# Optimization experiments

Measured on AMD Instinct MI355X. Metric: run time of the kernel, lower is better.

## Reference

```python
import jax, jax.numpy as jnp
import numpy as np

D_G, D_2D, D_3D = 512, 768, 1024
D_F, RANK, ATTN_H = 256, 16, 512
B = 8192


def _xavier(key, shape):
    fan_out, fan_in = shape
    lim = float(np.sqrt(6.0 / (fan_in + fan_out)))
    return jax.random.uniform(key, shape, jnp.float32, -lim, lim)


def setup_inputs() -> dict:
    key = jax.random.key(0)
    ks = jax.random.split(key, 12)
    inp = {
        "h_g": jax.random.normal(ks[0], (B, D_G), jnp.float32),
        "h_2d": jax.random.normal(ks[1], (B, D_2D), jnp.float32),
        "h_3d": jax.random.normal(ks[2], (B, D_3D), jnp.float32),
        # modality projections (torch Linear: y = x @ W.T + b)
        "Wg": _xavier(ks[3], (D_F, D_G)),   "bg": jnp.zeros((D_F,), jnp.float32),
        "W2": _xavier(ks[4], (D_F, D_2D)),  "b2": jnp.zeros((D_F,), jnp.float32),
        "W3": _xavier(ks[5], (D_F, D_3D)),  "b3": jnp.zeros((D_F,), jnp.float32),
        # LayerNorm affine params
        "ln_g_w": jnp.ones((D_F,), jnp.float32),  "ln_g_b": jnp.zeros((D_F,), jnp.float32),
        "ln_2_w": jnp.ones((D_F,), jnp.float32),  "ln_2_b": jnp.zeros((D_F,), jnp.float32),
        "ln_3_w": jnp.ones((D_F,), jnp.float32),  "ln_3_b": jnp.zeros((D_F,), jnp.float32),
        # rank expansions (no bias)
        "U": _xavier(ks[6], (RANK * D_F, D_F)),
        "V": _xavier(ks[7], (RANK * D_F, D_F)),
        "S": _xavier(ks[8], (RANK * D_F, D_F)),
        # attention MLP
        "Wa1": _xavier(ks[9], (ATTN_H, D_G + D_2D + D_3D)), "ba1": jnp.zeros((ATTN_H,), jnp.float32),
        "Wa2": _xavier(ks[10], (RANK, ATTN_H)),             "ba2": jnp.zeros((RANK,), jnp.float32),
    }
    return inp


def _layernorm(x, w, b, eps=1e-5):
    mu = jnp.mean(x, axis=-1, keepdims=True)
    var = jnp.var(x, axis=-1, keepdims=True)
    return (x - mu) * jax.lax.rsqrt(var + eps) * w + b


def reference(h_g, h_2d, h_3d, Wg, bg, W2, b2, W3, b3,
              ln_g_w, ln_g_b, ln_2_w, ln_2_b, ln_3_w, ln_3_b,
              U, V, S, Wa1, ba1, Wa2, ba2):
    # proj + LN + ReLU (dropout=0 / eval mode)
    g = jax.nn.relu(_layernorm(h_g @ Wg.T + bg, ln_g_w, ln_g_b))
    d2 = jax.nn.relu(_layernorm(h_2d @ W2.T + b2, ln_2_w, ln_2_b))
    d3 = jax.nn.relu(_layernorm(h_3d @ W3.T + b3, ln_3_w, ln_3_b))
    b = g.shape[0]
    # rank expansion: (B, R, d_f)
    g_r = (g @ U.T).reshape(b, RANK, D_F)
    d2_r = (d2 @ V.T).reshape(b, RANK, D_F)
    d3_r = (d3 @ S.T).reshape(b, RANK, D_F)
    z_r = g_r * d2_r * d3_r  # elementwise tri-linear product
    # rank attention from raw modality concat
    h_cat = jnp.concatenate([h_g, h_2d, h_3d], axis=-1)
    beta = jax.nn.softmax(jax.nn.relu(h_cat @ Wa1.T + ba1) @ Wa2.T + ba2, axis=-1)  # (B, R)
    z = jnp.einsum('brd,br->bd', z_r, beta)  # (B, d_f)
    return z
```

## Files before the change

kernel.cpp:

```cpp
#include <hip/hip_runtime.h>
#include <stdint.h>

#define B_ROWS 8192
#define DG 512
#define D2 768
#define D3 1024
#define DCAT 2304
#define DF 256
#define RANK 16
#define AH 512

#define OFF_WG 0
#define OFF_W2 131072
#define OFF_W3 327680
#define OFF_U  589824
#define OFF_V  1638400
#define OFF_S  2686976
#define OFF_WA1 3735552

#define WS_WBUF  0u
#define WS_HCAT  9830400u
#define WS_GBUF  9830400u
#define WS_PROJ  47579136u
#define WS_A1ACC 72744960u
#define WS_BETA  89522176u
#define WS_ZPART 47579136u
#define WS_REQUIRED 94240768u

typedef __attribute__((ext_vector_type(8))) short short8;
typedef __attribute__((ext_vector_type(4))) float f32x4;

__device__ inline unsigned short f2bf(float f) {
  union { float f; unsigned int u; } v; v.f = f;
  unsigned int u = v.u + 0x7fffu + ((v.u >> 16) & 1u);
  return (unsigned short)(u >> 16);
}
__device__ inline float bf2f(unsigned short h) {
  union { float f; unsigned int u; } v; v.u = ((unsigned int)h) << 16;
  return v.f;
}

typedef const unsigned int __attribute__((address_space(1)))* as1_u32p;
typedef unsigned int __attribute__((address_space(3)))* as3_u32p;

__device__ inline void g2l16(const unsigned short* g, unsigned short* l) {
  __builtin_amdgcn_global_load_lds((as1_u32p)g, (as3_u32p)l, 16, 0, 0);
}


__global__ __launch_bounds__(256) void cvt_hcat_k(const float* __restrict__ hg,
                                                  const float* __restrict__ h2,
                                                  const float* __restrict__ h3,
                                                  unsigned short* __restrict__ hcat) {
  const int idx = blockIdx.x * 256 + threadIdx.x;
  const int e = idx * 4;
  const int row = e / DCAT;
  const int col = e - row * DCAT;
  const float* src;
  if (col < DG) src = hg + (size_t)row * DG + col;
  else if (col < DG + D2) src = h2 + (size_t)row * D2 + (col - DG);
  else src = h3 + (size_t)row * D3 + (col - DG - D2);
  float4 v = *(const float4*)src;
  ushort4 o;
  o.x = f2bf(v.x); o.y = f2bf(v.y); o.z = f2bf(v.z); o.w = f2bf(v.w);
  *(ushort4*)(hcat + e) = o;
}

__global__ __launch_bounds__(256) void cvt_weights_k(const float* __restrict__ Wg,
                                                     const float* __restrict__ W2,
                                                     const float* __restrict__ W3,
                                                     const float* __restrict__ U,
                                                     const float* __restrict__ V,
                                                     const float* __restrict__ S,
                                                     const float* __restrict__ Wa1,
                                                     unsigned short* __restrict__ wbuf) {
  const int idx = blockIdx.x * 256 + threadIdx.x;
  const int e = idx * 4;
  const float* src;
  if (e < OFF_W2)       src = Wg  + e;
  else if (e < OFF_W3)  src = W2  + (e - OFF_W2);
  else if (e < OFF_U)   src = W3  + (e - OFF_W3);
  else if (e < OFF_V)   src = U   + (e - OFF_U);
  else if (e < OFF_S)   src = V   + (e - OFF_V);
  else if (e < OFF_WA1) src = S   + (e - OFF_S);
  else                  src = Wa1 + (e - OFF_WA1);
  float4 v = *(const float4*)src;
  ushort4 o;
  o.x = f2bf(v.x); o.y = f2bf(v.y); o.z = f2bf(v.z); o.w = f2bf(v.w);
  *(ushort4*)(wbuf + e) = o;
}


__device__ __forceinline__ void gemm_mainloop(const unsigned short* Ag, int lda,
                                              const unsigned short* Bg, int ldb,
                                              int K,
                                              unsigned short* lA, unsigned short* lB,
                                              f32x4 acc[4][4]) {
  const int tid = threadIdx.x;
  const int lane = tid & 63;
  const int wr = tid >> 7;
  const int wc = (tid >> 6) & 1;
#pragma unroll
  for (int i = 0; i < 4; ++i)
#pragma unroll
    for (int j = 0; j < 4; ++j)
      acc[i][j] = (f32x4){0.f, 0.f, 0.f, 0.f};

  const int row_s = tid >> 3;
  const int kc_s = (((tid & 7) ^ ((tid >> 3) & 7)) << 3);
  const int mbase = wr * 64 + (lane & 15);
  const int nbase = wc * 64 + (lane & 15);
  const int kq = lane >> 4;
  const int h = lane & 7;

  const int nsteps = K >> 6;
  for (int ks = 0; ks < nsteps; ++ks) {
    const int k0 = ks << 6;
    __syncthreads();
#pragma unroll
    for (int p = 0; p < 4; ++p) {
      const int row = p * 32 + row_s;
      const int lofs = (p * 256 + tid) * 8;
      g2l16(Ag + (size_t)row * lda + k0 + kc_s, lA + lofs);
      g2l16(Bg + (size_t)row * ldb + k0 + kc_s, lB + lofs);
    }
    __syncthreads();
#pragma unroll
    for (int kk = 0; kk < 2; ++kk) {
      const int kch = (kk << 2) + kq;
      const int ko = ((kch ^ h) << 3);
      short8 af[4], bfr[4];
#pragma unroll
      for (int t = 0; t < 4; ++t) {
        af[t]  = *(const short8*)(lA + (mbase + t * 16) * 64 + ko);
        bfr[t] = *(const short8*)(lB + (nbase + t * 16) * 64 + ko);
      }
#pragma unroll
      for (int ti = 0; ti < 4; ++ti)
#pragma unroll
        for (int tj = 0; tj < 4; ++tj)
          acc[ti][tj] = __builtin_amdgcn_mfma_f32_16x16x32_bf16(af[ti], bfr[tj], acc[ti][tj], 0, 0, 0);
    }
  }
}


__global__ __launch_bounds__(256) void fatgemm_k(const unsigned short* __restrict__ hcat,
                                                 const unsigned short* __restrict__ wbuf,
                                                 float* __restrict__ proj,
                                                 float* __restrict__ a1acc) {
  __shared__ __align__(16) unsigned short lA[128 * 64];
  __shared__ __align__(16) unsigned short lB[128 * 64];
  const int bid = blockIdx.x;
  f32x4 acc[4][4];
  const int lane = threadIdx.x & 63;
  const int wr = threadIdx.x >> 7, wc = (threadIdx.x >> 6) & 1;

  if (bid < 384) {
    const int z = bid >> 7;
    const int local = bid & 127;
    const int m0 = (local >> 1) << 7;
    const int n0 = (local & 1) << 7;
    const int Kz   = (z == 0) ? DG : (z == 1 ? D2 : D3);
    const int aoff = (z == 0) ? 0  : (z == 1 ? DG : DG + D2);
    const int woff = (z == 0) ? OFF_WG : (z == 1 ? OFF_W2 : OFF_W3);
    gemm_mainloop(hcat + (size_t)m0 * DCAT + aoff, DCAT,
                  wbuf + woff + (size_t)n0 * Kz, Kz, Kz, lA, lB, acc);
    float* out = proj + (size_t)z * B_ROWS * DF;
    const int r0 = m0 + wr * 64 + ((lane >> 4) << 2);
    const int c0 = n0 + wc * 64 + (lane & 15);
#pragma unroll
    for (int ti = 0; ti < 4; ++ti)
#pragma unroll
      for (int tj = 0; tj < 4; ++tj)
#pragma unroll
        for (int i = 0; i < 4; ++i)
          out[(size_t)(r0 + ti * 16 + i) * DF + (c0 + tj * 16)] = acc[ti][tj][i];
  } else {
    const int local = bid - 384;
    const int m0 = (local >> 2) << 7;
    const int n0 = (local & 3) << 7;
    gemm_mainloop(hcat + (size_t)m0 * DCAT, DCAT,
                  wbuf + OFF_WA1 + (size_t)n0 * DCAT, DCAT, DCAT, lA, lB, acc);
    const int r0 = m0 + wr * 64 + ((lane >> 4) << 2);
    const int c0 = n0 + wc * 64 + (lane & 15);
#pragma unroll
    for (int ti = 0; ti < 4; ++ti)
#pragma unroll
      for (int tj = 0; tj < 4; ++tj)
#pragma unroll
        for (int i = 0; i < 4; ++i)
          a1acc[(size_t)(r0 + ti * 16 + i) * AH + (c0 + tj * 16)] = acc[ti][tj][i];
  }
}


__global__ __launch_bounds__(256) void rank_fused_k(const unsigned short* __restrict__ gbuf,
                                                    const unsigned short* __restrict__ wbuf,
                                                    const float* __restrict__ beta,
                                                    float* __restrict__ zpart) {
  __shared__ __align__(16) unsigned short lA[128 * 64];
  __shared__ __align__(16) unsigned short lB[128 * 64];
  __shared__ float lbeta[4 * 128];
  const int m0 = blockIdx.x * 128;
  const int d0 = blockIdx.y * 128;
  const int rg = blockIdx.z * 4;

  for (int i = threadIdx.x; i < 512; i += 256) {
    const int rr = i >> 7, row = i & 127;
    lbeta[i] = beta[(size_t)(m0 + row) * RANK + rg + rr];
  }

  const int lane = threadIdx.x & 63;
  const int wr = threadIdx.x >> 7, wc = (threadIdx.x >> 6) & 1;
  const int lr0 = wr * 64 + ((lane >> 4) << 2);

  f32x4 zacc[4][4];
#pragma unroll
  for (int ti = 0; ti < 4; ++ti)
#pragma unroll
    for (int tj = 0; tj < 4; ++tj)
      zacc[ti][tj] = (f32x4){0.f, 0.f, 0.f, 0.f};

  for (int rr = 0; rr < 4; ++rr) {
    const int n0 = (rg + rr) * 256 + d0;
    f32x4 prod[4][4];
    f32x4 acc[4][4];
#pragma unroll
    for (int zi = 0; zi < 3; ++zi) {
      gemm_mainloop(gbuf + (size_t)zi * B_ROWS * DF + (size_t)m0 * DF, DF,
                    wbuf + OFF_U + (size_t)zi * 1048576 + (size_t)n0 * DF, DF, DF,
                    lA, lB, acc);
      if (zi == 0) {
#pragma unroll
        for (int ti = 0; ti < 4; ++ti)
#pragma unroll
          for (int tj = 0; tj < 4; ++tj)
            prod[ti][tj] = acc[ti][tj];
      } else {
#pragma unroll
        for (int ti = 0; ti < 4; ++ti)
#pragma unroll
          for (int tj = 0; tj < 4; ++tj)
            prod[ti][tj] *= acc[ti][tj];
      }
    }
#pragma unroll
    for (int ti = 0; ti < 4; ++ti) {
      const float4 b4 = *(const float4*)(lbeta + rr * 128 + lr0 + ti * 16);
      const float bv[4] = {b4.x, b4.y, b4.z, b4.w};
#pragma unroll
      for (int tj = 0; tj < 4; ++tj)
#pragma unroll
        for (int i = 0; i < 4; ++i)
          zacc[ti][tj][i] += prod[ti][tj][i] * bv[i];
    }
  }

  float* zp = zpart + (size_t)blockIdx.z * (B_ROWS * DF);
  const int c0 = d0 + wc * 64 + (lane & 15);
#pragma unroll
  for (int ti = 0; ti < 4; ++ti)
#pragma unroll
    for (int tj = 0; tj < 4; ++tj)
#pragma unroll
      for (int i = 0; i < 4; ++i)
        zp[(size_t)(m0 + lr0 + ti * 16 + i) * DF + (c0 + tj * 16)] = zacc[ti][tj][i];
}


__global__ __launch_bounds__(256) void zsum_k(const float* __restrict__ zpart,
                                              float* __restrict__ z) {
  const int idx = blockIdx.x * 256 + threadIdx.x;
  const size_t e = (size_t)idx * 4;
  const size_t stride = (size_t)B_ROWS * DF;
  float4 a = *(const float4*)(zpart + e);
  float4 b = *(const float4*)(zpart + stride + e);
  float4 c = *(const float4*)(zpart + 2 * stride + e);
  float4 d = *(const float4*)(zpart + 3 * stride + e);
  float4 o;
  o.x = (a.x + b.x) + (c.x + d.x);
  o.y = (a.y + b.y) + (c.y + d.y);
  o.z = (a.z + b.z) + (c.z + d.z);
  o.w = (a.w + b.w) + (c.w + d.w);
  *(float4*)(z + e) = o;
}


__global__ __launch_bounds__(256) void ln_relu_k(const float* __restrict__ proj,
                                                 const float* __restrict__ bg, const float* __restrict__ b2, const float* __restrict__ b3,
                                                 const float* __restrict__ wg, const float* __restrict__ wbg,
                                                 const float* __restrict__ w2, const float* __restrict__ wb2,
                                                 const float* __restrict__ w3, const float* __restrict__ wb3,
                                                 unsigned short* __restrict__ gout) {
  const int gid = blockIdx.x * 4 + (threadIdx.x >> 6);
  const int lane = threadIdx.x & 63;
  const int z = gid >> 13;
  const int row = gid & (B_ROWS - 1);
  const float* bias = z == 0 ? bg : (z == 1 ? b2 : b3);
  const float* lw = z == 0 ? wg : (z == 1 ? w2 : w3);
  const float* lb = z == 0 ? wbg : (z == 1 ? wb2 : wb3);
  const float* x = proj + (size_t)z * B_ROWS * DF + (size_t)row * DF + lane * 4;
  float4 v = *(const float4*)x;
  float4 bb = *(const float4*)(bias + lane * 4);
  v.x += bb.x; v.y += bb.y; v.z += bb.z; v.w += bb.w;
  float s = v.x + v.y + v.z + v.w;
  float q = v.x * v.x + v.y * v.y + v.z * v.z + v.w * v.w;
#pragma unroll
  for (int m = 1; m < 64; m <<= 1) { s += __shfl_xor(s, m, 64); q += __shfl_xor(q, m, 64); }
  const float mean = s * (1.f / DF);
  const float var = q * (1.f / DF) - mean * mean;
  const float rs = rsqrtf(var + 1e-5f);
  float4 w4 = *(const float4*)(lw + lane * 4);
  float4 b4 = *(const float4*)(lb + lane * 4);
  ushort4 o;
  o.x = f2bf(fmaxf((v.x - mean) * rs * w4.x + b4.x, 0.f));
  o.y = f2bf(fmaxf((v.y - mean) * rs * w4.y + b4.y, 0.f));
  o.z = f2bf(fmaxf((v.z - mean) * rs * w4.z + b4.z, 0.f));
  o.w = f2bf(fmaxf((v.w - mean) * rs * w4.w + b4.w, 0.f));
  *(ushort4*)(gout + (size_t)z * B_ROWS * DF + (size_t)row * DF + lane * 4) = o;
}


__global__ __launch_bounds__(256) void attn_beta_k(const float* __restrict__ a1acc,
                                                   const float* __restrict__ ba1,
                                                   const float* __restrict__ Wa2,
                                                   const float* __restrict__ ba2,
                                                   float* __restrict__ beta) {
  __shared__ float lw[RANK * AH];
  for (int i = threadIdx.x; i < RANK * AH / 4; i += 256)
    *(float4*)(lw + i * 4) = *(const float4*)(Wa2 + i * 4);
  __syncthreads();
  const int row = blockIdx.x * 4 + (threadIdx.x >> 6);
  const int lane = threadIdx.x & 63;
  const float* arow = a1acc + (size_t)row * AH + lane * 8;
  float4 aa = *(const float4*)arow;
  float4 ab = *(const float4*)(arow + 4);
  float4 ca = *(const float4*)(ba1 + lane * 8);
  float4 cb = *(const float4*)(ba1 + lane * 8 + 4);
  float av[8];
  av[0] = fmaxf(aa.x + ca.x, 0.f); av[1] = fmaxf(aa.y + ca.y, 0.f);
  av[2] = fmaxf(aa.z + ca.z, 0.f); av[3] = fmaxf(aa.w + ca.w, 0.f);
  av[4] = fmaxf(ab.x + cb.x, 0.f); av[5] = fmaxf(ab.y + cb.y, 0.f);
  av[6] = fmaxf(ab.z + cb.z, 0.f); av[7] = fmaxf(ab.w + cb.w, 0.f);
  float lg[RANK];
#pragma unroll
  for (int r = 0; r < RANK; ++r) {
    const float* wrow = lw + r * AH + lane * 8;
    float4 wa = *(const float4*)wrow;
    float4 wb = *(const float4*)(wrow + 4);
    float p = av[0] * wa.x + av[1] * wa.y + av[2] * wa.z + av[3] * wa.w
            + av[4] * wb.x + av[5] * wb.y + av[6] * wb.z + av[7] * wb.w;
#pragma unroll
    for (int m = 1; m < 64; m <<= 1) p += __shfl_xor(p, m, 64);
    lg[r] = p + ba2[r];
  }
  float mx = lg[0];
#pragma unroll
  for (int r = 1; r < RANK; ++r) mx = fmaxf(mx, lg[r]);
  float den = 0.f;
#pragma unroll
  for (int r = 0; r < RANK; ++r) { lg[r] = __expf(lg[r] - mx); den += lg[r]; }
  const float inv = 1.f / den;
  if (lane < RANK) {
    float mine = 0.f;
#pragma unroll
    for (int r = 0; r < RANK; ++r) mine = (lane == r) ? lg[r] : mine;
    beta[(size_t)row * RANK + lane] = mine * inv;
  }
}


extern "C" void kernel_launch(void* const* d_in, const int* in_sizes, int n_in,
                              void* d_out, int out_size, void* d_ws, size_t ws_size,
                              hipStream_t stream) {
  if (ws_size < (size_t)WS_REQUIRED) return;

  const float* h_g   = (const float*)d_in[0];
  const float* h_2d  = (const float*)d_in[1];
  const float* h_3d  = (const float*)d_in[2];
  const float* Wg    = (const float*)d_in[3];
  const float* bg    = (const float*)d_in[4];
  const float* W2    = (const float*)d_in[5];
  const float* b2    = (const float*)d_in[6];
  const float* W3    = (const float*)d_in[7];
  const float* b3    = (const float*)d_in[8];
  const float* ln_g_w = (const float*)d_in[9];
  const float* ln_g_b = (const float*)d_in[10];
  const float* ln_2_w = (const float*)d_in[11];
  const float* ln_2_b = (const float*)d_in[12];
  const float* ln_3_w = (const float*)d_in[13];
  const float* ln_3_b = (const float*)d_in[14];
  const float* U     = (const float*)d_in[15];
  const float* V     = (const float*)d_in[16];
  const float* S     = (const float*)d_in[17];
  const float* Wa1   = (const float*)d_in[18];
  const float* ba1   = (const float*)d_in[19];
  const float* Wa2   = (const float*)d_in[20];
  const float* ba2   = (const float*)d_in[21];

  char* ws = (char*)d_ws;
  unsigned short* wbuf  = (unsigned short*)(ws + WS_WBUF);
  unsigned short* hcat  = (unsigned short*)(ws + WS_HCAT);
  unsigned short* gbuf  = (unsigned short*)(ws + WS_GBUF);
  float*          proj  = (float*)(ws + WS_PROJ);
  float*          a1acc = (float*)(ws + WS_A1ACC);
  float*          beta  = (float*)(ws + WS_BETA);
  float*          zpart = (float*)(ws + WS_ZPART);
  float* z = (float*)d_out;

  cvt_hcat_k<<<dim3(18432), dim3(256), 0, stream>>>(h_g, h_2d, h_3d, hcat);
  cvt_weights_k<<<dim3(4800), dim3(256), 0, stream>>>(Wg, W2, W3, U, V, S, Wa1, wbuf);
  fatgemm_k<<<dim3(640), dim3(256), 0, stream>>>(hcat, wbuf, proj, a1acc);
  ln_relu_k<<<dim3(6144), dim3(256), 0, stream>>>(proj, bg, b2, b3, ln_g_w, ln_g_b,
                                                  ln_2_w, ln_2_b, ln_3_w, ln_3_b, gbuf);
  attn_beta_k<<<dim3(2048), dim3(256), 0, stream>>>(a1acc, ba1, Wa2, ba2, beta);
  rank_fused_k<<<dim3(64, 2, 4), dim3(256), 0, stream>>>(gbuf, wbuf, beta, zpart);
  zsum_k<<<dim3(2048), dim3(256), 0, stream>>>(zpart, z);
}
```

Before: 349.1 us.

## Split attention GEMM over K, fuse conversion kernels, use BK=128 rank mainloop

Merges the input and weight bf16 conversion kernels into one launch. Splits the long K=2304 attention-hidden GEMM into two halves so it runs as more, shorter tiles, with the partial results stored as bf16 and summed in attn_beta_k. The rank expansion GEMM now uses a K-tile of 128, which halves its loop iterations and barriers but doubles its LDS footprint. Storing partials in bf16 rounds them before they are summed, which costs some accuracy.

```diff
diff --git a/kernel.cpp b/kernel.cpp
--- a/kernel.cpp
+++ b/kernel.cpp
@@ -22,7 +22,7 @@
 #define WS_HCAT  9830400u
 #define WS_GBUF  9830400u
 #define WS_PROJ  47579136u
-#define WS_A1ACC 72744960u
+#define WS_A1P   72744960u
 #define WS_BETA  89522176u
 #define WS_ZPART 47579136u
 #define WS_REQUIRED 94240768u
@@ -48,46 +48,48 @@
 }
 
 
-__global__ __launch_bounds__(256) void cvt_hcat_k(const float* __restrict__ hg,
-                                                  const float* __restrict__ h2,
-                                                  const float* __restrict__ h3,
-                                                  unsigned short* __restrict__ hcat) {
-  const int idx = blockIdx.x * 256 + threadIdx.x;
-  const int e = idx * 4;
-  const int row = e / DCAT;
-  const int col = e - row * DCAT;
-  const float* src;
-  if (col < DG) src = hg + (size_t)row * DG + col;
-  else if (col < DG + D2) src = h2 + (size_t)row * D2 + (col - DG);
-  else src = h3 + (size_t)row * D3 + (col - DG - D2);
-  float4 v = *(const float4*)src;
-  ushort4 o;
-  o.x = f2bf(v.x); o.y = f2bf(v.y); o.z = f2bf(v.z); o.w = f2bf(v.w);
-  *(ushort4*)(hcat + e) = o;
-}
-
-__global__ __launch_bounds__(256) void cvt_weights_k(const float* __restrict__ Wg,
-                                                     const float* __restrict__ W2,
-                                                     const float* __restrict__ W3,
-                                                     const float* __restrict__ U,
-                                                     const float* __restrict__ V,
-                                                     const float* __restrict__ S,
-                                                     const float* __restrict__ Wa1,
-                                                     unsigned short* __restrict__ wbuf) {
-  const int idx = blockIdx.x * 256 + threadIdx.x;
-  const int e = idx * 4;
-  const float* src;
-  if (e < OFF_W2)       src = Wg  + e;
-  else if (e < OFF_W3)  src = W2  + (e - OFF_W2);
-  else if (e < OFF_U)   src = W3  + (e - OFF_W3);
-  else if (e < OFF_V)   src = U   + (e - OFF_U);
-  else if (e < OFF_S)   src = V   + (e - OFF_V);
-  else if (e < OFF_WA1) src = S   + (e - OFF_S);
-  else                  src = Wa1 + (e - OFF_WA1);
-  float4 v = *(const float4*)src;
-  ushort4 o;
-  o.x = f2bf(v.x); o.y = f2bf(v.y); o.z = f2bf(v.z); o.w = f2bf(v.w);
-  *(ushort4*)(wbuf + e) = o;
+__global__ __launch_bounds__(256) void cvt_all_k(const float* __restrict__ hg,
+                                                 const float* __restrict__ h2,
+                                                 const float* __restrict__ h3,
+                                                 const float* __restrict__ Wg,
+                                                 const float* __restrict__ W2,
+                                                 const float* __restrict__ W3,
+                                                 const float* __restrict__ U,
+                                                 const float* __restrict__ V,
+                                                 const float* __restrict__ S,
+                                                 const float* __restrict__ Wa1,
+                                                 unsigned short* __restrict__ hcat,
+                                                 unsigned short* __restrict__ wbuf) {
+  const int bid = blockIdx.x;
+  if (bid < 18432) {
+    const int idx = bid * 256 + threadIdx.x;
+    const int e = idx * 4;
+    const int row = e / DCAT;
+    const int col = e - row * DCAT;
+    const float* src;
+    if (col < DG) src = hg + (size_t)row * DG + col;
+    else if (col < DG + D2) src = h2 + (size_t)row * D2 + (col - DG);
+    else src = h3 + (size_t)row * D3 + (col - DG - D2);
+    float4 v = *(const float4*)src;
+    ushort4 o;
+    o.x = f2bf(v.x); o.y = f2bf(v.y); o.z = f2bf(v.z); o.w = f2bf(v.w);
+    *(ushort4*)(hcat + e) = o;
+  } else {
+    const int idx = (bid - 18432) * 256 + threadIdx.x;
+    const int e = idx * 4;
+    const float* src;
+    if (e < OFF_W2)       src = Wg  + e;
+    else if (e < OFF_W3)  src = W2  + (e - OFF_W2);
+    else if (e < OFF_U)   src = W3  + (e - OFF_W3);
+    else if (e < OFF_V)   src = U   + (e - OFF_U);
+    else if (e < OFF_S)   src = V   + (e - OFF_V);
+    else if (e < OFF_WA1) src = S   + (e - OFF_S);
+    else                  src = Wa1 + (e - OFF_WA1);
+    float4 v = *(const float4*)src;
+    ushort4 o;
+    o.x = f2bf(v.x); o.y = f2bf(v.y); o.z = f2bf(v.z); o.w = f2bf(v.w);
+    *(ushort4*)(wbuf + e) = o;
+  }
 }
 
 
@@ -145,10 +147,64 @@
 }
 
 
+__device__ __forceinline__ void gemm_mainloop_bk128(const unsigned short* Ag, int lda,
+                                                    const unsigned short* Bg, int ldb,
+                                                    int K,
+                                                    unsigned short* lA, unsigned short* lB,
+                                                    f32x4 acc[4][4]) {
+  const int tid = threadIdx.x;
+  const int lane = tid & 63;
+  const int wr = tid >> 7;
+  const int wc = (tid >> 6) & 1;
+#pragma unroll
+  for (int i = 0; i < 4; ++i)
+#pragma unroll
+    for (int j = 0; j < 4; ++j)
+      acc[i][j] = (f32x4){0.f, 0.f, 0.f, 0.f};
+
+  const int row_s = tid >> 4;
+  const int kc_s = (((tid & 15) ^ ((tid >> 4) & 15)) << 3);
+  const int mbase = wr * 64 + (lane & 15);
+  const int nbase = wc * 64 + (lane & 15);
+  const int kq = lane >> 4;
+  const int h = lane & 15;
+
+  const int nsteps = K >> 7;
+  for (int ks = 0; ks < nsteps; ++ks) {
+    const int k0 = ks << 7;
+    __syncthreads();
+#pragma unroll
+    for (int p = 0; p < 8; ++p) {
+      const int row = p * 16 + row_s;
+      const int lofs = (p * 256 + tid) * 8;
+      g2l16(Ag + (size_t)row * lda + k0 + kc_s, lA + lofs);
+      g2l16(Bg + (size_t)row * ldb + k0 + kc_s, lB + lofs);
+    }
+    __syncthreads();
+#pragma unroll
+    for (int kk = 0; kk < 4; ++kk) {
+      const int kch = (kk << 2) + kq;
+      const int ko = ((kch ^ h) << 3);
+      short8 af[4], bfr[4];
+#pragma unroll
+      for (int t = 0; t < 4; ++t) {
+        af[t]  = *(const short8*)(lA + (mbase + t * 16) * 128 + ko);
+        bfr[t] = *(const short8*)(lB + (nbase + t * 16) * 128 + ko);
+      }
+#pragma unroll
+      for (int ti = 0; ti < 4; ++ti)
+#pragma unroll
+        for (int tj = 0; tj < 4; ++tj)
+          acc[ti][tj] = __builtin_amdgcn_mfma_f32_16x16x32_bf16(af[ti], bfr[tj], acc[ti][tj], 0, 0, 0);
+    }
+  }
+}
+
+
 __global__ __launch_bounds__(256) void fatgemm_k(const unsigned short* __restrict__ hcat,
                                                  const unsigned short* __restrict__ wbuf,
                                                  float* __restrict__ proj,
-                                                 float* __restrict__ a1acc) {
+                                                 unsigned short* __restrict__ a1part) {
   __shared__ __align__(16) unsigned short lA[128 * 64];
   __shared__ __align__(16) unsigned short lB[128 * 64];
   const int bid = blockIdx.x;
@@ -177,11 +233,15 @@
         for (int i = 0; i < 4; ++i)
           out[(size_t)(r0 + ti * 16 + i) * DF + (c0 + tj * 16)] = acc[ti][tj][i];
   } else {
-    const int local = bid - 384;
+    const int t = bid - 384;
+    const int half = t >> 8;
+    const int local = t & 255;
     const int m0 = (local >> 2) << 7;
     const int n0 = (local & 3) << 7;
-    gemm_mainloop(hcat + (size_t)m0 * DCAT, DCAT,
-                  wbuf + OFF_WA1 + (size_t)n0 * DCAT, DCAT, DCAT, lA, lB, acc);
+    const int koff = half * 1152;
+    gemm_mainloop(hcat + (size_t)m0 * DCAT + koff, DCAT,
+                  wbuf + OFF_WA1 + (size_t)n0 * DCAT + koff, DCAT, 1152, lA, lB, acc);
+    unsigned short* out = a1part + (size_t)half * (B_ROWS * AH);
     const int r0 = m0 + wr * 64 + ((lane >> 4) << 2);
     const int c0 = n0 + wc * 64 + (lane & 15);
 #pragma unroll
@@ -190,7 +250,7 @@
       for (int tj = 0; tj < 4; ++tj)
 #pragma unroll
         for (int i = 0; i < 4; ++i)
-          a1acc[(size_t)(r0 + ti * 16 + i) * AH + (c0 + tj * 16)] = acc[ti][tj][i];
+          out[(size_t)(r0 + ti * 16 + i) * AH + (c0 + tj * 16)] = f2bf(acc[ti][tj][i]);
   }
 }
 
@@ -199,8 +259,8 @@
                                                     const unsigned short* __restrict__ wbuf,
                                                     const float* __restrict__ beta,
                                                     float* __restrict__ zpart) {
-  __shared__ __align__(16) unsigned short lA[128 * 64];
-  __shared__ __align__(16) unsigned short lB[128 * 64];
+  __shared__ __align__(16) unsigned short lA[128 * 128];
+  __shared__ __align__(16) unsigned short lB[128 * 128];
   __shared__ float lbeta[4 * 128];
   const int m0 = blockIdx.x * 128;
   const int d0 = blockIdx.y * 128;
@@ -228,9 +288,9 @@
     f32x4 acc[4][4];
 #pragma unroll
     for (int zi = 0; zi < 3; ++zi) {
-      gemm_mainloop(gbuf + (size_t)zi * B_ROWS * DF + (size_t)m0 * DF, DF,
-                    wbuf + OFF_U + (size_t)zi * 1048576 + (size_t)n0 * DF, DF, DF,
-                    lA, lB, acc);
+      gemm_mainloop_bk128(gbuf + (size_t)zi * B_ROWS * DF + (size_t)m0 * DF, DF,
+                          wbuf + OFF_U + (size_t)zi * 1048576 + (size_t)n0 * DF, DF, DF,
+                          lA, lB, acc);
       if (zi == 0) {
 #pragma unroll
         for (int ti = 0; ti < 4; ++ti)
@@ -322,7 +382,7 @@
 }
 
 
-__global__ __launch_bounds__(256) void attn_beta_k(const float* __restrict__ a1acc,
+__global__ __launch_bounds__(256) void attn_beta_k(const unsigned short* __restrict__ a1part,
                                                    const float* __restrict__ ba1,
                                                    const float* __restrict__ Wa2,
                                                    const float* __restrict__ ba2,
@@ -333,16 +393,23 @@
   __syncthreads();
   const int row = blockIdx.x * 4 + (threadIdx.x >> 6);
   const int lane = threadIdx.x & 63;
-  const float* arow = a1acc + (size_t)row * AH + lane * 8;
-  float4 aa = *(const float4*)arow;
-  float4 ab = *(const float4*)(arow + 4);
+  const unsigned short* h0 = a1part + (size_t)row * AH + lane * 8;
+  const unsigned short* h1 = h0 + (size_t)B_ROWS * AH;
+  const uint4 p0 = *(const uint4*)h0;
+  const uint4 p1 = *(const uint4*)h1;
+  const unsigned int u0[4] = {p0.x, p0.y, p0.z, p0.w};
+  const unsigned int u1[4] = {p1.x, p1.y, p1.z, p1.w};
   float4 ca = *(const float4*)(ba1 + lane * 8);
   float4 cb = *(const float4*)(ba1 + lane * 8 + 4);
+  const float bias[8] = {ca.x, ca.y, ca.z, ca.w, cb.x, cb.y, cb.z, cb.w};
   float av[8];
-  av[0] = fmaxf(aa.x + ca.x, 0.f); av[1] = fmaxf(aa.y + ca.y, 0.f);
-  av[2] = fmaxf(aa.z + ca.z, 0.f); av[3] = fmaxf(aa.w + ca.w, 0.f);
-  av[4] = fmaxf(ab.x + cb.x, 0.f); av[5] = fmaxf(ab.y + cb.y, 0.f);
-  av[6] = fmaxf(ab.z + cb.z, 0.f); av[7] = fmaxf(ab.w + cb.w, 0.f);
+#pragma unroll
+  for (int j = 0; j < 4; ++j) {
+    const float s0 = bf2f((unsigned short)(u0[j] & 0xffffu)) + bf2f((unsigned short)(u1[j] & 0xffffu));
+    const float s1 = bf2f((unsigned short)(u0[j] >> 16)) + bf2f((unsigned short)(u1[j] >> 16));
+    av[2 * j]     = fmaxf(s0 + bias[2 * j], 0.f);
+    av[2 * j + 1] = fmaxf(s1 + bias[2 * j + 1], 0.f);
+  }
   float lg[RANK];
 #pragma unroll
   for (int r = 0; r < RANK; ++r) {
@@ -400,21 +467,21 @@
   const float* ba2   = (const float*)d_in[21];
 
   char* ws = (char*)d_ws;
-  unsigned short* wbuf  = (unsigned short*)(ws + WS_WBUF);
-  unsigned short* hcat  = (unsigned short*)(ws + WS_HCAT);
-  unsigned short* gbuf  = (unsigned short*)(ws + WS_GBUF);
-  float*          proj  = (float*)(ws + WS_PROJ);
-  float*          a1acc = (float*)(ws + WS_A1ACC);
-  float*          beta  = (float*)(ws + WS_BETA);
-  float*          zpart = (float*)(ws + WS_ZPART);
+  unsigned short* wbuf   = (unsigned short*)(ws + WS_WBUF);
+  unsigned short* hcat   = (unsigned short*)(ws + WS_HCAT);
+  unsigned short* gbuf   = (unsigned short*)(ws + WS_GBUF);
+  float*          proj   = (float*)(ws + WS_PROJ);
+  unsigned short* a1part = (unsigned short*)(ws + WS_A1P);
+  float*          beta   = (float*)(ws + WS_BETA);
+  float*          zpart  = (float*)(ws + WS_ZPART);
   float* z = (float*)d_out;
 
-  cvt_hcat_k<<<dim3(18432), dim3(256), 0, stream>>>(h_g, h_2d, h_3d, hcat);
-  cvt_weights_k<<<dim3(4800), dim3(256), 0, stream>>>(Wg, W2, W3, U, V, S, Wa1, wbuf);
-  fatgemm_k<<<dim3(640), dim3(256), 0, stream>>>(hcat, wbuf, proj, a1acc);
+  cvt_all_k<<<dim3(23232), dim3(256), 0, stream>>>(h_g, h_2d, h_3d,
+                                                   Wg, W2, W3, U, V, S, Wa1, hcat, wbuf);
+  fatgemm_k<<<dim3(896), dim3(256), 0, stream>>>(hcat, wbuf, proj, a1part);
   ln_relu_k<<<dim3(6144), dim3(256), 0, stream>>>(proj, bg, b2, b3, ln_g_w, ln_g_b,
                                                   ln_2_w, ln_2_b, ln_3_w, ln_3_b, gbuf);
-  attn_beta_k<<<dim3(2048), dim3(256), 0, stream>>>(a1acc, ba1, Wa2, ba2, beta);
+  attn_beta_k<<<dim3(2048), dim3(256), 0, stream>>>(a1part, ba1, Wa2, ba2, beta);
   rank_fused_k<<<dim3(64, 2, 4), dim3(256), 0, stream>>>(gbuf, wbuf, beta, zpart);
   zsum_k<<<dim3(2048), dim3(256), 0, stream>>>(zpart, z);
 }
```

Result: faster. 324.6 us (-7.0%).
